# Kernel optimization log

Measured on AMD Instinct MI355X. Metric: run time of the kernel, lower is better.

## Reference

```python
import jax, jax.numpy as jnp
import numpy as np

EMB_DIM = 768
QKV_DIM = 64
NUM_HEAD = 12


def setup_inputs() -> dict:
    key = jax.random.key(0)
    k1, k2, k3 = jax.random.split(key, 3)
    z = jax.random.normal(k1, (16, 1024, EMB_DIM), dtype=jnp.float32)
    U_qkv = jax.random.normal(k2, (NUM_HEAD, 3, EMB_DIM, QKV_DIM), dtype=jnp.float32) * (1.0 / np.sqrt(EMB_DIM))
    U_msa = jax.random.normal(k3, (NUM_HEAD * QKV_DIM, EMB_DIM), dtype=jnp.float32) * (1.0 / np.sqrt(NUM_HEAD * QKV_DIM))
    return {"z": z, "U_qkv": U_qkv, "U_msa": U_msa}


def reference(z, U_qkv, U_msa):
    # z: [b, n, e]; U_qkv: [h, 3, e, d]; U_msa: [h*d, e]
    qkv = jnp.einsum("bne,hked->khbnd", z, U_qkv)  # [3, h, b, n, d]
    q, k, v = qkv[0], qkv[1], qkv[2]               # each [h, b, n, d]
    scale = 1.0 / jnp.sqrt(jnp.asarray(q.shape[-1], dtype=z.dtype))
    logits = jnp.einsum("hbnd,hbmd->hbnm", q, k) * scale  # [h, b, n, n]
    attn = jax.nn.softmax(logits, axis=-1)
    o = jnp.einsum("hbnm,hbmd->bnhd", attn, v)     # [b, n, h, d]
    b, n = o.shape[0], o.shape[1]
    o = o.reshape(b, n, -1)                        # [b, n, h*d]
    return o @ U_msa                               # [b, n, e]
```

## Files before the change

### kernel.cpp

```cpp
#include <hip/hip_runtime.h>
#include <hip/hip_bf16.h>

typedef _Float16 f16x8 __attribute__((ext_vector_type(8)));
typedef _Float16 f16x4 __attribute__((ext_vector_type(4)));
typedef float f32x4 __attribute__((ext_vector_type(4)));

#define MFMA32(a, b, c) __builtin_amdgcn_mfma_f32_16x16x32_f16(a, b, c, 0, 0, 0)
#define MFMA16(a, b, c) __builtin_amdgcn_mfma_f32_16x16x16f16(a, b, c, 0, 0, 0)

#define GLOAD_LDS16(g, l)                                         \
  __builtin_amdgcn_global_load_lds(                               \
      (const __attribute__((address_space(1))) void*)(g),         \
      (__attribute__((address_space(3))) void*)(l), 16, 0, 0)

__global__ __launch_bounds__(256) void tconv_kernel(
    const float* __restrict__ in, _Float16* __restrict__ out, int R, int C) {
  size_t bat = (size_t)blockIdx.y * R * C;
  int o = blockIdx.x * 256 + threadIdx.x;
  if (o < R * C) {
    int c = o / R, r = o - c * R;
    out[bat + o] = (_Float16)in[bat + (size_t)r * C + c];
  }
}

__global__ __launch_bounds__(256) void cvt16_kernel(
    const float* __restrict__ in, _Float16* __restrict__ out, int n) {
  int i = (blockIdx.x * 256 + threadIdx.x) * 8;
  if (i < n) {
    float4 a = *(const float4*)(in + i);
    float4 b = *(const float4*)(in + i + 4);
    f16x8 cv;
    cv[0] = (_Float16)a.x; cv[1] = (_Float16)a.y;
    cv[2] = (_Float16)a.z; cv[3] = (_Float16)a.w;
    cv[4] = (_Float16)b.x; cv[5] = (_Float16)b.y;
    cv[6] = (_Float16)b.z; cv[7] = (_Float16)b.w;
    *(f16x8*)(out + i) = cv;
  }
}

__global__ __launch_bounds__(256) void qkv_gemm_kernel(
    const _Float16* __restrict__ zh, const _Float16* __restrict__ Ut,
    _Float16* __restrict__ Qf, _Float16* __restrict__ Kf,
    _Float16* __restrict__ Vt) {
  __shared__ _Float16 As[2][128 * 64];
  __shared__ _Float16 Bs[2][128 * 64];

  const int tid = threadIdx.x;
  const int wv = tid >> 6, lane = tid & 63, quad = lane >> 4, l16 = lane & 15;

  const int m0 = blockIdx.x * 128;
  const int by = blockIdx.y;
  const int n0 = by * 128;

  const int srow = lane >> 3;
  const int scol = ((lane & 7) ^ srow) << 3;
  const _Float16* Ag = zh + (size_t)(m0 + srow) * 768 + scol;
  const _Float16* Bg = Ut + (size_t)(n0 + srow) * 768 + scol;

  const int cbq = quad * 16;

  f32x4 acc[2][8] = {};

#pragma unroll
  for (int i = 0; i < 4; ++i) {
    const int rb = (i * 4 + wv) * 8;
    GLOAD_LDS16(Ag + (size_t)rb * 768, (char*)As[0] + rb * 128);
    GLOAD_LDS16(Bg + (size_t)rb * 768, (char*)Bs[0] + rb * 128);
  }
  asm volatile("s_waitcnt vmcnt(0)" ::: "memory");
  __builtin_amdgcn_s_barrier();

  for (int t = 0; t < 12; ++t) {
    const int cur = t & 1;
    if (t < 11) {
      const int k1 = (t + 1) * 64;
#pragma unroll
      for (int i = 0; i < 4; ++i) {
        const int rb = (i * 4 + wv) * 8;
        GLOAD_LDS16(Ag + (size_t)rb * 768 + k1,
                    (char*)As[cur ^ 1] + rb * 128);
        GLOAD_LDS16(Bg + (size_t)rb * 768 + k1,
                    (char*)Bs[cur ^ 1] + rb * 128);
      }
    }
#pragma unroll
    for (int ks = 0; ks < 2; ++ks) {
      f16x8 af[2], bfr[8];
#pragma unroll
      for (int rt = 0; rt < 2; ++rt) {
        const int r = wv * 32 + rt * 16 + l16;
        af[rt] = *(const f16x8*)((const char*)As[cur] + r * 128 +
                                 ((ks * 64 + cbq) ^ ((r & 7) << 4)));
      }
#pragma unroll
      for (int ct = 0; ct < 8; ++ct) {
        const int r = ct * 16 + l16;
        bfr[ct] = *(const f16x8*)((const char*)Bs[cur] + r * 128 +
                                  ((ks * 64 + cbq) ^ ((r & 7) << 4)));
      }
#pragma unroll
      for (int rt = 0; rt < 2; ++rt)
#pragma unroll
        for (int ct = 0; ct < 8; ++ct)
          acc[rt][ct] = MFMA32(af[rt], bfr[ct], acc[rt][ct]);
    }
    if (t < 11) {
      asm volatile("s_waitcnt vmcnt(0)" ::: "memory");
      __builtin_amdgcn_s_barrier();
    }
  }

#pragma unroll
  for (int ct = 0; ct < 8; ++ct) {
    const int g = by * 2 + (ct >> 2);
    const int h = g / 3, kk = g - h * 3;
    const int dd = (ct & 3) * 16 + l16;
#pragma unroll
    for (int rt = 0; rt < 2; ++rt) {
#pragma unroll
      for (int r = 0; r < 4; ++r) {
        int m = m0 + wv * 32 + rt * 16 + quad * 4 + r;
        int b = m >> 10, n = m & 1023;
        _Float16 val = (_Float16)acc[rt][ct][r];
        if (kk == 0)
          Qf[(((size_t)h * 16 + b) * 1024 + n) * 64 + dd] = val;
        else if (kk == 1)
          Kf[(((size_t)h * 16 + b) * 1024 + n) * 64 + dd] = val;
        else
          Vt[(((size_t)h * 16 + b) * 64 + dd) * 1024 + n] = val;
      }
    }
  }
}

__global__ __launch_bounds__(256) void attn_kernel(
    const _Float16* __restrict__ Qf, const _Float16* __restrict__ Kf,
    const _Float16* __restrict__ Vt, _Float16* __restrict__ Of) {
  __shared__ _Float16 Ks[2][64][72];
  __shared__ _Float16 Vs[2][64][72];

  const int tid = threadIdx.x;
  const int wv = tid >> 6, lane = tid & 63, quad = lane >> 4, l16 = lane & 15;

  const int flat = blockIdx.x;
  const int swz = (flat & 7) * 192 + (flat >> 3);
  const int hb = swz >> 3;
  const int h = hb >> 4, b = hb & 15;
  const _Float16* Q = Qf + (size_t)hb * 65536;
  const _Float16* K = Kf + (size_t)hb * 65536;
  const _Float16* V = Vt + (size_t)hb * 65536;
  const int q0 = (swz & 7) * 128 + wv * 32;

  const _Float16 cs = (_Float16)0.18033688011112042f;
  f16x8 qfr[2][2];
#pragma unroll
  for (int mi = 0; mi < 2; ++mi) {
    const _Float16* qp = Q + (size_t)(q0 + mi * 16 + l16) * 64 + quad * 8;
    qfr[mi][0] = *(const f16x8*)qp * cs;
    qfr[mi][1] = *(const f16x8*)(qp + 32) * cs;
  }

  const int r0 = tid >> 3, c0 = (tid & 7) << 3;
  const _Float16* Kst = K + (size_t)r0 * 64 + c0;
  const _Float16* Vst = V + (size_t)r0 * 1024 + c0;

  uint4 kreg[2], vreg[2];
#pragma unroll
  for (int i = 0; i < 2; ++i) {
    kreg[i] = *(const uint4*)(Kst + i * 2048);
    vreg[i] = *(const uint4*)(Vst + i * 32768);
  }
#pragma unroll
  for (int i = 0; i < 2; ++i) {
    *(uint4*)&Ks[0][r0 + i * 32][c0] = kreg[i];
    *(uint4*)&Vs[0][r0 + i * 32][c0] = vreg[i];
  }
  __syncthreads();

  f32x4 o[2][4] = {};
  float lsum[2] = {};

  for (int t = 0; t < 16; ++t) {
    const int cur = t & 1;
    if (t < 15) {
      int n1 = (t + 1) * 64;
#pragma unroll
      for (int i = 0; i < 2; ++i) {
        kreg[i] = *(const uint4*)(Kst + (size_t)n1 * 64 + i * 2048);
        vreg[i] = *(const uint4*)(Vst + n1 + i * 32768);
      }
    }

    f32x4 st[2][4] = {};
    __builtin_amdgcn_s_setprio(1);
#pragma unroll
    for (int ct = 0; ct < 4; ++ct) {
      f16x8 kf0 = *(const f16x8*)&Ks[cur][ct * 16 + l16][quad * 8];
      f16x8 kf1 = *(const f16x8*)&Ks[cur][ct * 16 + l16][32 + quad * 8];
#pragma unroll
      for (int mi = 0; mi < 2; ++mi) {
        st[mi][ct] = MFMA32(kf0, qfr[mi][0], st[mi][ct]);
        st[mi][ct] = MFMA32(kf1, qfr[mi][1], st[mi][ct]);
      }
    }
    __builtin_amdgcn_s_setprio(0);

    f16x4 pa[2][4];
#pragma unroll
    for (int mi = 0; mi < 2; ++mi)
#pragma unroll
      for (int ct = 0; ct < 4; ++ct)
#pragma unroll
        for (int r = 0; r < 4; ++r) {
          float p = __builtin_amdgcn_exp2f(st[mi][ct][r]);
          lsum[mi] += p;
          pa[mi][ct][r] = (_Float16)p;
        }

    __builtin_amdgcn_s_setprio(1);
#pragma unroll
    for (int dt = 0; dt < 4; ++dt) {
#pragma unroll
      for (int kb = 0; kb < 4; ++kb) {
        f16x4 vf = *(const f16x4*)&Vs[cur][dt * 16 + l16][kb * 16 + quad * 4];
#pragma unroll
        for (int mi = 0; mi < 2; ++mi)
          o[mi][dt] = MFMA16(pa[mi][kb], vf, o[mi][dt]);
      }
    }
    __builtin_amdgcn_s_setprio(0);

    if (t < 15) {
#pragma unroll
      for (int i = 0; i < 2; ++i) {
        *(uint4*)&Ks[cur ^ 1][r0 + i * 32][c0] = kreg[i];
        *(uint4*)&Vs[cur ^ 1][r0 + i * 32][c0] = vreg[i];
      }
      __syncthreads();
    }
  }

#pragma unroll
  for (int mi = 0; mi < 2; ++mi) {
    float s = lsum[mi];
    s += __shfl_xor(s, 16, 64);
    s += __shfl_xor(s, 32, 64);
    lsum[mi] = s;
  }

#pragma unroll
  for (int mi = 0; mi < 2; ++mi) {
#pragma unroll
    for (int r = 0; r < 4; ++r) {
      float inv = 1.f / __shfl(lsum[mi], quad * 4 + r, 64);
      int n = q0 + mi * 16 + quad * 4 + r;
#pragma unroll
      for (int dt = 0; dt < 4; ++dt) {
        int dd = dt * 16 + l16;
        __builtin_nontemporal_store(
            (_Float16)(o[mi][dt][r] * inv),
            &Of[((size_t)b * 1024 + n) * 768 + h * 64 + dd]);
      }
    }
  }
}

__global__ __launch_bounds__(256) void out_gemm_kernel(
    const _Float16* __restrict__ A, const _Float16* __restrict__ Bt,
    float* __restrict__ Cout) {
  __shared__ _Float16 As[2][128 * 64];
  __shared__ _Float16 Bs[2][128 * 64];

  const int tid = threadIdx.x;
  const int wv = tid >> 6, lane = tid & 63, quad = lane >> 4, l16 = lane & 15;

  const int m0 = blockIdx.x * 128;
  const int n0 = blockIdx.y * 128;

  const int srow = lane >> 3;
  const int scol = ((lane & 7) ^ srow) << 3;
  const _Float16* Ag = A + (size_t)(m0 + srow) * 768 + scol;
  const _Float16* Bg = Bt + (size_t)(n0 + srow) * 768 + scol;

  const int cbq = quad * 16;

  f32x4 acc[2][8] = {};

#pragma unroll
  for (int i = 0; i < 4; ++i) {
    const int rb = (i * 4 + wv) * 8;
    GLOAD_LDS16(Ag + (size_t)rb * 768, (char*)As[0] + rb * 128);
    GLOAD_LDS16(Bg + (size_t)rb * 768, (char*)Bs[0] + rb * 128);
  }
  asm volatile("s_waitcnt vmcnt(0)" ::: "memory");
  __builtin_amdgcn_s_barrier();

  for (int t = 0; t < 12; ++t) {
    const int cur = t & 1;
    if (t < 11) {
      const int k1 = (t + 1) * 64;
#pragma unroll
      for (int i = 0; i < 4; ++i) {
        const int rb = (i * 4 + wv) * 8;
        GLOAD_LDS16(Ag + (size_t)rb * 768 + k1,
                    (char*)As[cur ^ 1] + rb * 128);
        GLOAD_LDS16(Bg + (size_t)rb * 768 + k1,
                    (char*)Bs[cur ^ 1] + rb * 128);
      }
    }
#pragma unroll
    for (int ks = 0; ks < 2; ++ks) {
      f16x8 af[2], bfr[8];
#pragma unroll
      for (int rt = 0; rt < 2; ++rt) {
        const int r = wv * 32 + rt * 16 + l16;
        af[rt] = *(const f16x8*)((const char*)As[cur] + r * 128 +
                                 ((ks * 64 + cbq) ^ ((r & 7) << 4)));
      }
#pragma unroll
      for (int ct = 0; ct < 8; ++ct) {
        const int r = ct * 16 + l16;
        bfr[ct] = *(const f16x8*)((const char*)Bs[cur] + r * 128 +
                                  ((ks * 64 + cbq) ^ ((r & 7) << 4)));
      }
#pragma unroll
      for (int rt = 0; rt < 2; ++rt)
#pragma unroll
        for (int ct = 0; ct < 8; ++ct)
          acc[rt][ct] = MFMA32(af[rt], bfr[ct], acc[rt][ct]);
    }
    if (t < 11) {
      asm volatile("s_waitcnt vmcnt(0)" ::: "memory");
      __builtin_amdgcn_s_barrier();
    }
  }

#pragma unroll
  for (int rt = 0; rt < 2; ++rt) {
#pragma unroll
    for (int ct = 0; ct < 8; ++ct) {
#pragma unroll
      for (int r = 0; r < 4; ++r) {
        int m = m0 + wv * 32 + rt * 16 + quad * 4 + r;
        int n = n0 + ct * 16 + l16;
        __builtin_nontemporal_store(acc[rt][ct][r],
                                    &Cout[(size_t)m * 768 + n]);
      }
    }
  }
}

extern "C" void kernel_launch(void* const* d_in, const int* in_sizes, int n_in,
                              void* d_out, int out_size, void* d_ws,
                              size_t ws_size, hipStream_t stream) {
  const float* z = (const float*)d_in[0];
  const float* Uqkv = (const float*)d_in[1];
  const float* Umsa = (const float*)d_in[2];

  char* ws = (char*)d_ws;
  _Float16* Ut_qkv = (_Float16*)(ws);
  _Float16* Ut_msa = (_Float16*)(ws + 3538944);
  _Float16* zh = (_Float16*)(ws + 4718592);
  _Float16* Of = zh;
  _Float16* Qf = (_Float16*)(ws + 29884416);
  _Float16* Kf = (_Float16*)(ws + 55050240);
  _Float16* Vt = (_Float16*)(ws + 80216064);

  tconv_kernel<<<dim3(192, 36), 256, 0, stream>>>(Uqkv, Ut_qkv, 768, 64);
  tconv_kernel<<<dim3(2304, 1), 256, 0, stream>>>(Umsa, Ut_msa, 768, 768);
  cvt16_kernel<<<dim3(6144, 1), 256, 0, stream>>>(z, zh, 16384 * 768);

  qkv_gemm_kernel<<<dim3(128, 18), 256, 0, stream>>>(zh, Ut_qkv, Qf, Kf, Vt);
  attn_kernel<<<dim3(1536, 1), 256, 0, stream>>>(Qf, Kf, Vt, Of);
  out_gemm_kernel<<<dim3(128, 6), 256, 0, stream>>>(Of, Ut_msa,
                                                    (float*)d_out);
}
```

Baseline: 347.6 us.

## Enlarge QKV GEMM tile to 256x256 with 8 waves and interleaved prefetch

The QKV projection GEMM now uses 256x256 output tiles computed by 512 threads (a 2x4 wave grid), with each wave owning a 128x64 sub-tile. Loads for the next K slice are split into quarters and issued between MFMA phases, and s_setprio raises wave priority around the MFMA blocks. The larger tile raises arithmetic intensity and cuts global traffic per output. In exchange it uses 128KB of LDS and more accumulator registers, and the grid shrinks to 576 blocks, which could hurt occupancy and load balance.

```diff
diff --git a/kernel.cpp b/kernel.cpp
--- a/kernel.cpp
+++ b/kernel.cpp
@@ -38,99 +38,118 @@
   }
 }
 
-__global__ __launch_bounds__(256) void qkv_gemm_kernel(
+__global__ __launch_bounds__(512) void qkv_gemm_kernel(
     const _Float16* __restrict__ zh, const _Float16* __restrict__ Ut,
     _Float16* __restrict__ Qf, _Float16* __restrict__ Kf,
     _Float16* __restrict__ Vt) {
-  __shared__ _Float16 As[2][128 * 64];
-  __shared__ _Float16 Bs[2][128 * 64];
+  __shared__ _Float16 As[2][256 * 64];
+  __shared__ _Float16 Bs[2][256 * 64];
 
   const int tid = threadIdx.x;
-  const int wv = tid >> 6, lane = tid & 63, quad = lane >> 4, l16 = lane & 15;
-
-  const int m0 = blockIdx.x * 128;
+  const int wid = tid >> 6, lane = tid & 63, quad = lane >> 4, l16 = lane & 15;
+  const int wr = wid >> 2, wc = wid & 3;
+
+  const int m0 = blockIdx.x * 256;
   const int by = blockIdx.y;
-  const int n0 = by * 128;
+  const int n0 = by * 256;
 
   const int srow = lane >> 3;
   const int scol = ((lane & 7) ^ srow) << 3;
   const _Float16* Ag = zh + (size_t)(m0 + srow) * 768 + scol;
   const _Float16* Bg = Ut + (size_t)(n0 + srow) * 768 + scol;
 
-  const int cbq = quad * 16;
-
-  f32x4 acc[2][8] = {};
-
-#pragma unroll
-  for (int i = 0; i < 4; ++i) {
-    const int rb = (i * 4 + wv) * 8;
-    GLOAD_LDS16(Ag + (size_t)rb * 768, (char*)As[0] + rb * 128);
-    GLOAD_LDS16(Bg + (size_t)rb * 768, (char*)Bs[0] + rb * 128);
-  }
-  asm volatile("s_waitcnt vmcnt(0)" ::: "memory");
-  __builtin_amdgcn_s_barrier();
+#define STAGE_A(buf, t)                                                  \
+  {                                                                      \
+    _Pragma("unroll") for (int hf = 0; hf < 2; ++hf)                     \
+        _Pragma("unroll") for (int i = 0; i < 2; ++i) {                  \
+      const int rb = hf * 128 + (wid * 2 + i) * 8;                       \
+      GLOAD_LDS16(Ag + (size_t)rb * 768 + (t) * 64,                      \
+                  (char*)&As[buf][0] + rb * 128);                        \
+    }                                                                    \
+  }
+#define STAGE_B(buf, t)                                                  \
+  {                                                                      \
+    _Pragma("unroll") for (int hf = 0; hf < 2; ++hf)                     \
+        _Pragma("unroll") for (int i = 0; i < 2; ++i) {                  \
+      const int rb = hf * 128 + (wid * 2 + i) * 8;                       \
+      GLOAD_LDS16(Bg + (size_t)rb * 768 + (t) * 64,                      \
+                  (char*)&Bs[buf][0] + rb * 128);                        \
+    }                                                                    \
+  }
+
+  f32x4 acc[8][4] = {};
+
+  STAGE_A(0, 0);
+  STAGE_B(0, 0);
 
   for (int t = 0; t < 12; ++t) {
     const int cur = t & 1;
-    if (t < 11) {
-      const int k1 = (t + 1) * 64;
-#pragma unroll
-      for (int i = 0; i < 4; ++i) {
-        const int rb = (i * 4 + wv) * 8;
-        GLOAD_LDS16(Ag + (size_t)rb * 768 + k1,
-                    (char*)As[cur ^ 1] + rb * 128);
-        GLOAD_LDS16(Bg + (size_t)rb * 768 + k1,
-                    (char*)Bs[cur ^ 1] + rb * 128);
-      }
-    }
-#pragma unroll
-    for (int ks = 0; ks < 2; ++ks) {
-      f16x8 af[2], bfr[8];
-#pragma unroll
-      for (int rt = 0; rt < 2; ++rt) {
-        const int r = wv * 32 + rt * 16 + l16;
-        af[rt] = *(const f16x8*)((const char*)As[cur] + r * 128 +
-                                 ((ks * 64 + cbq) ^ ((r & 7) << 4)));
-      }
-#pragma unroll
-      for (int ct = 0; ct < 8; ++ct) {
-        const int r = ct * 16 + l16;
-        bfr[ct] = *(const f16x8*)((const char*)Bs[cur] + r * 128 +
-                                  ((ks * 64 + cbq) ^ ((r & 7) << 4)));
-      }
-#pragma unroll
-      for (int rt = 0; rt < 2; ++rt)
-#pragma unroll
-        for (int ct = 0; ct < 8; ++ct)
-          acc[rt][ct] = MFMA32(af[rt], bfr[ct], acc[rt][ct]);
-    }
-    if (t < 11) {
-      asm volatile("s_waitcnt vmcnt(0)" ::: "memory");
-      __builtin_amdgcn_s_barrier();
-    }
-  }
-
-#pragma unroll
-  for (int ct = 0; ct < 8; ++ct) {
-    const int g = by * 2 + (ct >> 2);
-    const int h = g / 3, kk = g - h * 3;
-    const int dd = (ct & 3) * 16 + l16;
-#pragma unroll
-    for (int rt = 0; rt < 2; ++rt) {
+    asm volatile("s_waitcnt vmcnt(0)" ::: "memory");
+    asm volatile("s_barrier" ::: "memory");
+#pragma unroll
+    for (int q = 0; q < 4; ++q) {
+      const int mh = q >> 1, nh = q & 1;
+      f16x8 af[4][2], bf[2][2];
+#pragma unroll
+      for (int mf = 0; mf < 4; ++mf) {
+        const int r = wr * 128 + mh * 64 + mf * 16 + l16;
+#pragma unroll
+        for (int ks = 0; ks < 2; ++ks)
+          af[mf][ks] =
+              *(const f16x8*)((const char*)&As[cur][0] + r * 128 +
+                              ((ks * 64 + quad * 16) ^ ((r & 7) << 4)));
+      }
+#pragma unroll
+      for (int j = 0; j < 2; ++j) {
+        const int r = wc * 64 + nh * 32 + j * 16 + l16;
+#pragma unroll
+        for (int ks = 0; ks < 2; ++ks)
+          bf[j][ks] =
+              *(const f16x8*)((const char*)&Bs[cur][0] + r * 128 +
+                              ((ks * 64 + quad * 16) ^ ((r & 7) << 4)));
+      }
+      if (t < 11) {
+        if (q == 0) STAGE_A(cur ^ 1, t + 1)
+        else if (q == 1) STAGE_B(cur ^ 1, t + 1)
+      }
+      asm volatile("s_barrier" ::: "memory");
+      __builtin_amdgcn_s_setprio(1);
+#pragma unroll
+      for (int mf = 0; mf < 4; ++mf)
+#pragma unroll
+        for (int j = 0; j < 2; ++j)
+#pragma unroll
+          for (int ks = 0; ks < 2; ++ks)
+            acc[mh * 4 + mf][nh * 2 + j] =
+                MFMA32(af[mf][ks], bf[j][ks], acc[mh * 4 + mf][nh * 2 + j]);
+      __builtin_amdgcn_s_setprio(0);
+      asm volatile("s_barrier" ::: "memory");
+    }
+  }
+
+  const int g = by * 4 + wc;
+  const int hd = g / 3, kk = g - hd * 3;
+#pragma unroll
+  for (int mfp = 0; mfp < 8; ++mfp) {
+#pragma unroll
+    for (int nfp = 0; nfp < 4; ++nfp) {
+      const int dd = nfp * 16 + l16;
 #pragma unroll
       for (int r = 0; r < 4; ++r) {
-        int m = m0 + wv * 32 + rt * 16 + quad * 4 + r;
+        int m = m0 + wr * 128 + mfp * 16 + quad * 4 + r;
         int b = m >> 10, n = m & 1023;
-        _Float16 val = (_Float16)acc[rt][ct][r];
+        _Float16 val = (_Float16)acc[mfp][nfp][r];
         if (kk == 0)
-          Qf[(((size_t)h * 16 + b) * 1024 + n) * 64 + dd] = val;
+          Qf[(((size_t)hd * 16 + b) * 1024 + n) * 64 + dd] = val;
         else if (kk == 1)
-          Kf[(((size_t)h * 16 + b) * 1024 + n) * 64 + dd] = val;
+          Kf[(((size_t)hd * 16 + b) * 1024 + n) * 64 + dd] = val;
         else
-          Vt[(((size_t)h * 16 + b) * 64 + dd) * 1024 + n] = val;
-      }
-    }
-  }
+          Vt[(((size_t)hd * 16 + b) * 64 + dd) * 1024 + n] = val;
+      }
+    }
+  }
+#undef STAGE_A
+#undef STAGE_B
 }
 
 __global__ __launch_bounds__(256) void attn_kernel(
@@ -370,7 +389,7 @@
   tconv_kernel<<<dim3(2304, 1), 256, 0, stream>>>(Umsa, Ut_msa, 768, 768);
   cvt16_kernel<<<dim3(6144, 1), 256, 0, stream>>>(z, zh, 16384 * 768);
 
-  qkv_gemm_kernel<<<dim3(128, 18), 256, 0, stream>>>(zh, Ut_qkv, Qf, Kf, Vt);
+  qkv_gemm_kernel<<<dim3(64, 9), 512, 0, stream>>>(zh, Ut_qkv, Qf, Kf, Vt);
   attn_kernel<<<dim3(1536, 1), 256, 0, stream>>>(Qf, Kf, Vt, Of);
   out_gemm_kernel<<<dim3(128, 6), 256, 0, stream>>>(Of, Ut_msa,
                                                     (float*)d_out);
```

New measurement: 355.9 us. 2.4% more time.

## Replace double-buffered LDS pipeline in QKV GEMM with single-buffer loop

Applied to the files above, without the earlier changes.

The QKV projection GEMM drops its two-stage LDS ping-pong buffer. It now loads each 64-wide K tile into a single shared buffer between two __syncthreads barriers, then computes on it. This halves the shared memory per block, which may allow more resident blocks per CU. In exchange, global-to-LDS loads no longer overlap with MFMA compute, and each iteration adds an extra barrier.

```diff
diff --git a/kernel.cpp b/kernel.cpp
--- a/kernel.cpp
+++ b/kernel.cpp
@@ -42,8 +42,8 @@
     const _Float16* __restrict__ zh, const _Float16* __restrict__ Ut,
     _Float16* __restrict__ Qf, _Float16* __restrict__ Kf,
     _Float16* __restrict__ Vt) {
-  __shared__ _Float16 As[2][128 * 64];
-  __shared__ _Float16 Bs[2][128 * 64];
+  __shared__ _Float16 As[128 * 64];
+  __shared__ _Float16 Bs[128 * 64];
 
   const int tid = threadIdx.x;
   const int wv = tid >> 6, lane = tid & 63, quad = lane >> 4, l16 = lane & 15;
@@ -61,41 +61,28 @@
 
   f32x4 acc[2][8] = {};
 
-#pragma unroll
-  for (int i = 0; i < 4; ++i) {
-    const int rb = (i * 4 + wv) * 8;
-    GLOAD_LDS16(Ag + (size_t)rb * 768, (char*)As[0] + rb * 128);
-    GLOAD_LDS16(Bg + (size_t)rb * 768, (char*)Bs[0] + rb * 128);
-  }
-  asm volatile("s_waitcnt vmcnt(0)" ::: "memory");
-  __builtin_amdgcn_s_barrier();
-
-  for (int t = 0; t < 12; ++t) {
-    const int cur = t & 1;
-    if (t < 11) {
-      const int k1 = (t + 1) * 64;
-#pragma unroll
-      for (int i = 0; i < 4; ++i) {
-        const int rb = (i * 4 + wv) * 8;
-        GLOAD_LDS16(Ag + (size_t)rb * 768 + k1,
-                    (char*)As[cur ^ 1] + rb * 128);
-        GLOAD_LDS16(Bg + (size_t)rb * 768 + k1,
-                    (char*)Bs[cur ^ 1] + rb * 128);
-      }
-    }
+  for (int k0 = 0; k0 < 768; k0 += 64) {
+    __syncthreads();
+#pragma unroll
+    for (int i = 0; i < 4; ++i) {
+      const int rb = (i * 4 + wv) * 8;
+      GLOAD_LDS16(Ag + (size_t)rb * 768 + k0, (char*)As + rb * 128);
+      GLOAD_LDS16(Bg + (size_t)rb * 768 + k0, (char*)Bs + rb * 128);
+    }
+    __syncthreads();
 #pragma unroll
     for (int ks = 0; ks < 2; ++ks) {
       f16x8 af[2], bfr[8];
 #pragma unroll
       for (int rt = 0; rt < 2; ++rt) {
         const int r = wv * 32 + rt * 16 + l16;
-        af[rt] = *(const f16x8*)((const char*)As[cur] + r * 128 +
+        af[rt] = *(const f16x8*)((const char*)As + r * 128 +
                                  ((ks * 64 + cbq) ^ ((r & 7) << 4)));
       }
 #pragma unroll
       for (int ct = 0; ct < 8; ++ct) {
         const int r = ct * 16 + l16;
-        bfr[ct] = *(const f16x8*)((const char*)Bs[cur] + r * 128 +
+        bfr[ct] = *(const f16x8*)((const char*)Bs + r * 128 +
                                   ((ks * 64 + cbq) ^ ((r & 7) << 4)));
       }
 #pragma unroll
@@ -103,10 +90,6 @@
 #pragma unroll
         for (int ct = 0; ct < 8; ++ct)
           acc[rt][ct] = MFMA32(af[rt], bfr[ct], acc[rt][ct]);
-    }
-    if (t < 11) {
-      asm volatile("s_waitcnt vmcnt(0)" ::: "memory");
-      __builtin_amdgcn_s_barrier();
     }
   }
 
```

After: 353.5 us. Within noise of the previous version (+1.7%).
